# Optimization experiments

Hardware: AMD Instinct MI355X
Metric: run time of the kernel (lower is better)

Reference implementation:

```python
import jax, jax.numpy as jnp
import numpy as np

HEAD_DIM = 64
NORM_EPS = 1e-5
W_SCALE = -0.6065306597126334  # -exp(-0.5)


def _rwkv7_scan(r, w, k, v, a, b):
    # r,w,k,a,b: [B,T,H,K]; v: [B,T,H,V]. Official RWKV7 recurrence (per head):
    #   S_t = S_{t-1} * diag(exp(w_t)) + (S_{t-1} @ a_t) b_t^T + v_t k_t^T ,  o_t = S_t @ r_t
    Bsz, T, H, K = r.shape
    V = v.shape[-1]
    decay = jnp.exp(w)

    def step(S, xs):
        r_t, d_t, k_t, v_t, a_t, b_t = xs
        sa = jnp.einsum('bhvk,bhk->bhv', S, a_t)
        S = S * d_t[:, :, None, :] + sa[..., None] * b_t[:, :, None, :] + v_t[..., None] * k_t[:, :, None, :]
        o_t = jnp.einsum('bhvk,bhk->bhv', S, r_t)
        return S, o_t

    xs = tuple(jnp.moveaxis(t, 1, 0) for t in (r, decay, k, v, a, b))
    S0 = jnp.zeros((Bsz, H, V, K), dtype=r.dtype)
    _, o = jax.lax.scan(step, S0, xs)
    return jnp.moveaxis(o, 0, 1)  # [B,T,H,V]


def setup_inputs() -> dict:
    key = jax.random.key(0)
    B, T, H = 2, 4096, 2048
    NH, DK, DV = 32, 64, 64
    D_DECAY, D_A, D_V, D_G = 96, 96, 64, 256
    ks = iter(jax.random.split(key, 40))
    n = lambda *s: jax.random.normal(next(ks), s, dtype=jnp.float32)
    u = lambda *s: jax.random.uniform(next(ks), s, dtype=jnp.float32)
    inp = {
        'hidden_states': n(B, T, H),
        'v_first': n(B, T, H),
        'x_r': u(1, 1, H), 'x_w': u(1, 1, H), 'x_k': u(1, 1, H),
        'x_v': u(1, 1, H), 'x_a': u(1, 1, H), 'x_g': u(1, 1, H),
        'k_k': 0.71 + 0.05 * n(H),
        'k_a': 1.02 + 0.05 * n(H),
        'r_k': -0.04 + 0.02 * n(NH, DK),
        'w_r': 0.02 * n(H, H), 'w_k': 0.002 * n(H, H),
        'w_v': 0.02 * n(H, H), 'w_o': 0.02 * n(H, H),
        'wA': 0.02 * n(D_DECAY, H), 'wB': 0.02 * n(H, D_DECAY), 'wb': -0.5 + 0.1 * n(H),
        'aA': 0.02 * n(D_A, H), 'aB': 0.02 * n(H, D_A), 'ab': 0.1 * n(H),
        'vA': 0.02 * n(D_V, H), 'vB': 0.02 * n(H, D_V), 'vb': 0.5 + 0.1 * n(H),
        'gA': 0.02 * n(D_G, H), 'gB': 0.02 * n(H, D_G),
        'gn_w': jnp.ones(H, jnp.float32),
        'gn_b': jnp.zeros(H, jnp.float32),
    }
    return inp


def reference(hidden_states, v_first, x_r, x_w, x_k, x_v, x_a, x_g,
              k_k, k_a, r_k, w_r, w_k, w_v, w_o,
              wA, wB, wb, aA, aB, ab, vA, vB, vb, gA, gB, gn_w, gn_b):
    B, T, H = hidden_states.shape
    NH, DK = r_k.shape
    DV = H // NH
    # token shift: delta = shift(x) - x (zero-padded at t=0)
    shifted = jnp.pad(hidden_states, ((0, 0), (1, 0), (0, 0)))[:, :-1]
    delta = shifted - hidden_states
    xr = hidden_states + delta * x_r
    xw = hidden_states + delta * x_w
    xk = hidden_states + delta * x_k
    xv = hidden_states + delta * x_v
    xa = hidden_states + delta * x_a
    xg = hidden_states + delta * x_g
    r = xr @ w_r.T
    w = W_SCALE * jax.nn.sigmoid(jnp.tanh(xw @ wA.T) @ wB.T + wb)  # log-decay in (-0.6065, 0)
    k = xk @ w_k.T
    v = xv @ w_v.T
    v = v + (v_first - v) * jax.nn.sigmoid((xv @ vA.T) @ vB.T + vb)  # lerp with v_first (layer_idx != 0)
    a = jax.nn.sigmoid((xa @ aA.T) @ aB.T + ab)
    g = jax.nn.sigmoid(xg @ gA.T) @ gB.T  # g_lora: sigmoid activation inside, no bias
    kk = (k * k_k).reshape(B, T, NH, DK)
    kk = kk / jnp.maximum(jnp.linalg.norm(kk, axis=-1, keepdims=True), 1e-12)
    k = k * (1.0 + (a - 1.0) * k_a)  # fused_k_rwkv7
    r4 = r.reshape(B, T, NH, DK)
    w4 = w.reshape(B, T, NH, DK)
    k4 = k.reshape(B, T, NH, DK)
    a4 = a.reshape(B, T, NH, DK)
    v4 = v.reshape(B, T, NH, DV)
    o = _rwkv7_scan(r4, w4, k4, v4, -kk, kk * a4)  # [B,T,NH,DV]
    # GroupNorm over each head (eps = head_dim * norm_eps)
    mu = o.mean(-1, keepdims=True)
    var = ((o - mu) ** 2).mean(-1, keepdims=True)
    on = (o - mu) / jnp.sqrt(var + HEAD_DIM * NORM_EPS)
    on = on * gn_w.reshape(NH, DV) + gn_b.reshape(NH, DV)
    on = on + (r4 * k4 * r_k).sum(-1, keepdims=True) * v4
    out = (on.reshape(B, T, H) * g) @ w_o.T
    return out
```

## Files before the change

kernel.cpp:

```cpp
#include <hip/hip_runtime.h>
#include <cstdint>
#include <cstddef>

typedef unsigned short u16;
typedef unsigned int u32;

typedef __bf16 bf8_t __attribute__((ext_vector_type(8)));
typedef float f4_t __attribute__((ext_vector_type(4)));

__device__ __forceinline__ u16 f2bf(float x) {
  u32 u = __float_as_uint(x);
  u = (u + 0x7fffu + ((u >> 16) & 1u)) >> 16;
  return (u16)u;
}
__device__ __forceinline__ float bf2f(u16 x) {
  u32 u = ((u32)x) << 16;
  return __uint_as_float(u);
}
__device__ __forceinline__ float sigf(float x) { return 1.f / (1.f + __expf(-x)); }

#define MFMA16(a, b, c) __builtin_amdgcn_mfma_f32_16x16x32_bf16(a, b, c, 0, 0, 0)

__global__ void fill_kernel(float* p, float v, long n) {
  long i = (long)blockIdx.x * blockDim.x + threadIdx.x;
  if (i < n) p[i] = v;
}

__global__ void padcvt_kernel(const float* __restrict__ src, u16* __restrict__ dst,
                              int rows, int cols, int pc, long total) {
  long i = (long)blockIdx.x * blockDim.x + threadIdx.x;
  if (i >= total) return;
  int r = (int)(i / pc), c = (int)(i % pc);
  float v = (r < rows && c < cols) ? src[(long)r * cols + c] : 0.f;
  dst[i] = f2bf(v);
}

__global__ void wf_kernel(const float* __restrict__ src, const float* __restrict__ coef,
                          u16* __restrict__ Wf, int rows_valid, int row0, long total) {
  long i = (long)blockIdx.x * blockDim.x + threadIdx.x;
  if (i >= total) return;
  int r = (int)(i >> 12);
  int k = (int)(i & 4095);
  float v = 0.f;
  if (r < rows_valid) {
    int kk = k & 2047;
    v = src[(long)r * 2048 + kk];
    if (k >= 2048) v *= coef[kk];
  }
  Wf[(long)(row0 + r) * 4096 + k] = f2bf(v);
}

__global__ void wab_kernel(const float* __restrict__ wB, const float* __restrict__ aB,
                           u16* __restrict__ Wab, long total) {
  long i = (long)blockIdx.x * blockDim.x + threadIdx.x;
  if (i >= total) return;
  int r = (int)(i >> 8), k = (int)(i & 255);
  float v = 0.f;
  if (r < 2048) { if (k < 96) v = wB[(long)r * 96 + k]; }
  else { int rr = r - 2048; if (k >= 128 && k < 224) v = aB[(long)rr * 96 + (k - 128)]; }
  Wab[i] = f2bf(v);
}

__global__ void hd_kernel(const float* __restrict__ h_b, u16* __restrict__ out_seg,
                          int t0, int Tc, long total4) {
  long i = (long)blockIdx.x * blockDim.x + threadIdx.x;
  if (i >= total4) return;
  long e = i * 4;
  const int H = 2048;
  int col = (int)(e % H);
  int tl = (int)(e / H);
  int tg = t0 + tl;
  const float* hp = h_b + (long)tg * H + col;
  float4 hv = *(const float4*)hp;
  float4 pv = make_float4(0.f, 0.f, 0.f, 0.f);
  if (tg > 0) pv = *(const float4*)(hp - H);
  u16* row = out_seg + (long)tl * 4096;
  uint2 ph, pd;
  ph.x = (u32)f2bf(hv.x) | ((u32)f2bf(hv.y) << 16);
  ph.y = (u32)f2bf(hv.z) | ((u32)f2bf(hv.w) << 16);
  pd.x = (u32)f2bf(pv.x - hv.x) | ((u32)f2bf(pv.y - hv.y) << 16);
  pd.y = (u32)f2bf(pv.z - hv.z) | ((u32)f2bf(pv.w - hv.w) << 16);
  *(uint2*)(row + col) = ph;
  *(uint2*)(row + 2048 + col) = pd;
}

__global__ void mix1_kernel(const float* __restrict__ h_b, const float* __restrict__ coef,
                            u16* __restrict__ out_seg, int t0, int Tc, long total4) {
  long i = (long)blockIdx.x * blockDim.x + threadIdx.x;
  if (i >= total4) return;
  long e = i * 4;
  const int H = 2048;
  int col = (int)(e % H);
  int tl = (int)(e / H);
  int tg = t0 + tl;
  const float* hp = h_b + (long)tg * H + col;
  float4 hv = *(const float4*)hp;
  float4 pv = make_float4(0.f, 0.f, 0.f, 0.f);
  if (tg > 0) pv = *(const float4*)(hp - H);
  float4 cc = *(const float4*)(coef + col);
  uint2 pk;
  pk.x = (u32)f2bf(hv.x + (pv.x - hv.x) * cc.x) | ((u32)f2bf(hv.y + (pv.y - hv.y) * cc.y) << 16);
  pk.y = (u32)f2bf(hv.z + (pv.z - hv.z) * cc.z) | ((u32)f2bf(hv.w + (pv.w - hv.w) * cc.w) << 16);
  *(uint2*)(out_seg + e) = pk;
}

#define LDSW 40
template <int MODE>
__global__ __launch_bounds__(256) void gemm_bt(
    const u16* __restrict__ A, const u16* __restrict__ B, void* __restrict__ Cv,
    int M, int N, int K, int lda, const float* __restrict__ aux1) {
  __shared__ u16 sA[128 * LDSW];
  __shared__ u16 sB[128 * LDSW];
  const int tid = threadIdx.x;
  const long bm = (long)blockIdx.y * 128;
  const long bn = (long)blockIdx.x * 128;
  const int wave = tid >> 6, lane = tid & 63;
  const int wm = (wave >> 1) * 64, wn = (wave & 1) * 64;
  const int quad = lane >> 4, rr = lane & 15;

  f4_t acc[4][4];
  const f4_t zero = {0.f, 0.f, 0.f, 0.f};
#pragma unroll
  for (int i = 0; i < 4; i++)
#pragma unroll
    for (int j = 0; j < 4; j++) acc[i][j] = zero;

  const int c0 = tid, c1 = tid + 256;
  const u16* pa0 = A + (bm + (c0 >> 2)) * (long)lda + (c0 & 3) * 8;
  const u16* pa1 = A + (bm + (c1 >> 2)) * (long)lda + (c1 & 3) * 8;
  const u16* pb0 = B + (bn + (c0 >> 2)) * (long)K + (c0 & 3) * 8;
  const u16* pb1 = B + (bn + (c1 >> 2)) * (long)K + (c1 & 3) * 8;

  uint4 a0A, a1A, b0A, b1A, a0B, a1B, b0B, b1B;
#define LDGA(k0)                            \
  {                                         \
    a0A = *(const uint4*)(pa0 + (k0));      \
    a1A = *(const uint4*)(pa1 + (k0));      \
    b0A = *(const uint4*)(pb0 + (k0));      \
    b1A = *(const uint4*)(pb1 + (k0));      \
  }
#define LDGB(k0)                            \
  {                                         \
    a0B = *(const uint4*)(pa0 + (k0));      \
    a1B = *(const uint4*)(pa1 + (k0));      \
    b0B = *(const uint4*)(pb0 + (k0));      \
    b1B = *(const uint4*)(pb1 + (k0));      \
  }
#define STLDS(ra0, ra1, rb0, rb1)                          \
  {                                                        \
    *(uint4*)(&sA[(c0 >> 2) * LDSW + (c0 & 3) * 8]) = ra0; \
    *(uint4*)(&sA[(c1 >> 2) * LDSW + (c1 & 3) * 8]) = ra1; \
    *(uint4*)(&sB[(c0 >> 2) * LDSW + (c0 & 3) * 8]) = rb0; \
    *(uint4*)(&sB[(c1 >> 2) * LDSW + (c1 & 3) * 8]) = rb1; \
  }
#define COMPUTE                                                        \
  {                                                                    \
    bf8_t af[4], bfv[4];                                               \
    _Pragma("unroll") for (int i = 0; i < 4; i++)                      \
        af[i] = *(const bf8_t*)(&sA[(wm + i * 16 + rr) * LDSW + quad * 8]); \
    _Pragma("unroll") for (int j = 0; j < 4; j++)                      \
        bfv[j] = *(const bf8_t*)(&sB[(wn + j * 16 + rr) * LDSW + quad * 8]); \
    _Pragma("unroll") for (int i = 0; i < 4; i++)                      \
        _Pragma("unroll") for (int j = 0; j < 4; j++)                  \
            acc[i][j] = MFMA16(af[i], bfv[j], acc[i][j]);              \
  }

  LDGA(0);
  LDGB(32);
  for (int k0 = 0; k0 < K; k0 += 64) {
    __syncthreads();
    STLDS(a0A, a1A, b0A, b1A);
    __syncthreads();
    if (k0 + 64 < K) LDGA(k0 + 64);
    COMPUTE;
    __syncthreads();
    STLDS(a0B, a1B, b0B, b1B);
    __syncthreads();
    if (k0 + 96 < K) LDGB(k0 + 96);
    COMPUTE;
  }
#undef LDGA
#undef LDGB
#undef STLDS
#undef COMPUTE
#pragma unroll
  for (int i = 0; i < 4; i++)
#pragma unroll
    for (int j = 0; j < 4; j++)
#pragma unroll
      for (int rg = 0; rg < 4; rg++) {
        long m = bm + wm + i * 16 + quad * 4 + rg;
        long n = bn + wn + j * 16 + rr;
        long id = m * (long)N + n;
        float x = acc[i][j][rg];
        if (MODE == 0) ((float*)Cv)[id] = x;
        else if (MODE == 1) ((u16*)Cv)[id] = f2bf(x);
        else if (MODE == 2) ((u16*)Cv)[id] = f2bf(tanhf(x));
        else if (MODE == 3) ((u16*)Cv)[id] = f2bf(sigf(x));
        else if (MODE == 5) {
          float y = (n < 128) ? tanhf(x) : ((n < 384) ? x : sigf(x));
          ((u16*)Cv)[id] = f2bf(y);
        } else if (MODE == 6) {
          ((u16*)Cv)[id] = f2bf(sigf(x + aux1[(int)n]));
        }
      }
}

__device__ __forceinline__ void gload16(const u16* g, u16* l) {
  __builtin_amdgcn_global_load_lds((const __attribute__((address_space(1))) u32*)g,
                                   (__attribute__((address_space(3))) u32*)l, 16, 0, 0);
}

template <int MODE>
__global__ __launch_bounds__(512, 2) void gemm256_bt(
    const u16* __restrict__ A, const u16* __restrict__ Bw, void* __restrict__ Cv,
    int M, int N, int K, int rsp, long r0off, long r1off) {
  __shared__ u16 L[2][2][2][8192];
  const int tid = threadIdx.x;
  const int lane = tid & 63, w = tid >> 6;
  const int quad = lane >> 4, l15 = lane & 15;
  const long bm = (long)blockIdx.y * 256, bn = (long)blockIdx.x * 256;
  const int wm = (w >> 2) * 128, wn = (w & 3) * 64;
  const int NT = K >> 6;

  const int u0 = tid, u1 = tid + 512;
  const int ar0 = u0 >> 2, ar1 = u1 >> 2;
  const int aq0 = (u0 & 3) ^ (ar0 & 3), aq1 = (u1 & 3) ^ (ar1 & 3);
  const u16* gA0 = A + (bm + ar0) * (long)K + aq0 * 8;
  const u16* gA1 = A + (bm + ar1) * (long)K + aq1 * 8;
  const u16* gB0 = Bw + (bn + ar0) * (long)K + aq0 * 8;
  const u16* gB1 = Bw + (bn + ar1) * (long)K + aq1 * 8;

  const int qx = (quad ^ (l15 & 3)) * 8;
  const int roA = (wm + l15) * 32 + qx;
  const int roB = (wn + l15) * 32 + qx;

  f4_t acc[8][4];
#pragma unroll
  for (int i = 0; i < 8; i++)
#pragma unroll
    for (int j = 0; j < 4; j++) acc[i][j] = (f4_t){0.f, 0.f, 0.f, 0.f};

#define STG_A(buf, s, tt)                                   \
  {                                                         \
    long ko = ((long)(tt) << 6) + ((s) << 5);               \
    gload16(gA0 + ko, &L[buf][0][s][u0 * 8]);               \
    gload16(gA1 + ko, &L[buf][0][s][u1 * 8]);               \
  }
#define STG_B(buf, s, tt)                                   \
  {                                                         \
    long ko = ((long)(tt) << 6) + ((s) << 5);               \
    gload16(gB0 + ko, &L[buf][1][s][u0 * 8]);               \
    gload16(gB1 + ko, &L[buf][1][s][u1 * 8]);               \
  }
#define LDA4(P, o)                                          \
  _Pragma("unroll") for (int i = 0; i < 4; i++)             \
      aF[i] = *(const bf8_t*)((P) + roA + ((o) + i) * 512);
#define LDB4(P)                                             \
  _Pragma("unroll") for (int j = 0; j < 4; j++)             \
      bF[j] = *(const bf8_t*)((P) + roB + j * 512);
#define MFMA_BLK(base)                                      \
  __builtin_amdgcn_s_setprio(1);                            \
  _Pragma("unroll") for (int i = 0; i < 4; i++)             \
      _Pragma("unroll") for (int j = 0; j < 4; j++)         \
          acc[(base) + i][j] = MFMA16(aF[i], bF[j], acc[(base) + i][j]); \
  __builtin_amdgcn_s_setprio(0);
#define SBAR __builtin_amdgcn_s_barrier()

  STG_A(0, 0, 0); STG_B(0, 0, 0);
  STG_A(0, 1, 0); STG_B(0, 1, 0);
  if (NT > 1) { STG_A(1, 0, 1); STG_B(1, 0, 1); }
  asm volatile("s_waitcnt vmcnt(8)" ::: "memory");
  SBAR;

  bf8_t aF[4], bF[4];
  for (int t = 0; t < NT; ++t) {
    const int buf = t & 1;
    const u16* A0 = &L[buf][0][0][0];
    const u16* B0 = &L[buf][1][0][0];
    const u16* A1 = &L[buf][0][1][0];
    const u16* B1 = &L[buf][1][1][0];
    LDA4(A0, 0);
    LDB4(B0);
    if (t + 1 < NT) STG_A(buf ^ 1, 1, t + 1);
    SBAR;
    asm volatile("s_waitcnt lgkmcnt(0)" ::: "memory");
    MFMA_BLK(0);
    SBAR;
    LDA4(A0, 4);
    if (t + 1 < NT) STG_B(buf ^ 1, 1, t + 1);
    SBAR;
    asm volatile("s_waitcnt lgkmcnt(0)" ::: "memory");
    MFMA_BLK(4);
    if (t == NT - 1) asm volatile("s_waitcnt vmcnt(0)" ::: "memory");
    else asm volatile("s_waitcnt vmcnt(8)" ::: "memory");
    SBAR;
    LDA4(A1, 0);
    LDB4(B1);
    if (t + 2 < NT) STG_A(buf, 0, t + 2);
    SBAR;
    asm volatile("s_waitcnt lgkmcnt(0)" ::: "memory");
    MFMA_BLK(0);
    SBAR;
    LDA4(A1, 4);
    if (t + 2 < NT) STG_B(buf, 0, t + 2);
    SBAR;
    asm volatile("s_waitcnt lgkmcnt(0)" ::: "memory");
    MFMA_BLK(4);
    if (t == NT - 2) asm volatile("s_waitcnt vmcnt(4)" ::: "memory");
    else if (t < NT - 2) asm volatile("s_waitcnt vmcnt(8)" ::: "memory");
    SBAR;
  }

#pragma unroll
  for (int i = 0; i < 8; i++) {
#pragma unroll
    for (int rg = 0; rg < 4; rg++) {
      long mm = bm + wm + i * 16 + quad * 4 + rg;
      long crow = (mm < rsp) ? (mm + r0off) : (mm + r1off);
#pragma unroll
      for (int j = 0; j < 4; j++) {
        long n = bn + wn + j * 16 + l15;
        float x = acc[i][j][rg];
        if (MODE == 0) ((float*)Cv)[crow * (long)N + n] = x;
        else ((u16*)Cv)[crow * (long)N + n] = f2bf(x);
      }
    }
  }
#undef STG_A
#undef STG_B
#undef LDA4
#undef LDB4
#undef MFMA_BLK
#undef SBAR
}

__global__ __launch_bounds__(256) void post1_kernel(
    const float* __restrict__ F1, const float* __restrict__ F0F4, float* __restrict__ W,
    const float* __restrict__ F2, const u16* __restrict__ VL,
    const float* __restrict__ vfirst,
    u16* __restrict__ KM, u16* __restrict__ KK, u16* __restrict__ BB, u16* __restrict__ VB,
    const float* __restrict__ k_k, const float* __restrict__ k_a,
    const float* __restrict__ wb, const float* __restrict__ ab, int t0, int Tc) {
  const int lane = threadIdx.x & 63;
  const long th = (((long)blockIdx.x * 256) + threadIdx.x) >> 6;
  const int hcol = (int)(th & 31) * 64 + lane;
  const long idx = th * 64 + lane;
  const long r = th >> 5;
  float kraw = F1[idx];
  float kk0 = kraw * k_k[hcol];
  float ss = kk0 * kk0;
#pragma unroll
  for (int m = 32; m; m >>= 1) ss += __shfl_xor(ss, m, 64);
  float kkn = kk0 / fmaxf(sqrtf(ss), 1e-12f);
  float wlog = F0F4[r * 4096 + hcol];
  float alog = F0F4[r * 4096 + 2048 + hcol];
  float av = sigf(alog + ab[hcol]);
  float w = -0.6065306597126334f * sigf(wlog + wb[hcol]);
  W[idx] = w;
  KM[idx] = f2bf(kraw * (1.f + (av - 1.f) * k_a[hcol]));
  KK[idx] = f2bf(kkn);
  BB[idx] = f2bf(kkn * av);
  float vraw = F2[idx];
  float sg = bf2f(VL[idx]);
  long vfi = ((r / Tc) * 4096 + t0 + (r % Tc)) * 2048 + hcol;
  VB[idx] = f2bf(vraw + (vfirst[vfi] - vraw) * sg);
}

constexpr int ST64 = 72;
constexpr int ST32 = 40;
constexpr int STX = 132;

__global__ __launch_bounds__(64) void phaseA_kernel(
    const float* __restrict__ wS, const u16* __restrict__ kmS, const u16* __restrict__ kkS,
    const u16* __restrict__ bbS, const u16* __restrict__ vbS, const u16* __restrict__ rbS,
    float* __restrict__ POWb, u16* __restrict__ PAb, float* __restrict__ Zb,
    u16* __restrict__ GTb, float* __restrict__ CLb, int Tc, int sp0) {
  __shared__ u16 lXa[16 * ST64], lXr[16 * ST64], lYa[16 * ST64], lYb[16 * ST64];
  __shared__ u16 lYaT[64 * ST32], lYbT[64 * ST32], lVmT[64 * ST32];
  __shared__ u16 lTWt[64 * ST32], lTAt[64 * ST32];
  __shared__ u16 lP[16 * ST32], lQ[16 * ST32], lBm[16 * ST32];
  __shared__ float lA[16 * 16];
  __shared__ float lX[16 * STX];
  __shared__ float lcl[64];
  const int lane = threadIdx.x;
  const int quad = lane >> 4, l15 = lane & 15;
  const long tile = blockIdx.x;
  const int bh = (int)(tile & 63);
  const int col = (int)(tile >> 6);
  const int b = bh >> 5, h = bh & 31;
  const long s = tile;
  const f4_t z4 = {0.f, 0.f, 0.f, 0.f};

  {
    u32* p0 = (u32*)&lYaT[lane * ST32 + 16];
    u32* p1 = (u32*)&lYbT[lane * ST32 + 16];
    u32* p2 = (u32*)&lVmT[lane * ST32 + 16];
    u32* p3 = (u32*)&lTWt[lane * ST32 + 16];
    u32* p4 = (u32*)&lTAt[lane * ST32 + 16];
#pragma unroll
    for (int q = 0; q < 8; q++) { p0[q] = 0; p1[q] = 0; p2[q] = 0; p3[q] = 0; p4[q] = 0; }
    if (lane < 16) {
      u32* q0 = (u32*)&lP[lane * ST32 + 16];
      u32* q1 = (u32*)&lQ[lane * ST32 + 16];
      u32* q2 = (u32*)&lBm[lane * ST32 + 16];
#pragma unroll
      for (int q = 0; q < 8; q++) { q0[q] = 0; q1[q] = 0; q2[q] = 0; }
    }
  }

  const long rowbase = (long)b * Tc + (long)(sp0 + col) * 16;
  const long gbase = rowbase * 2048 + (long)h * 64 + lane;
  float cw = 0.f;
#pragma unroll
  for (int i = 0; i < 16; i++) {
    long g = gbase + (long)i * 2048;
    float w = wS[g];
    float km = bf2f(kmS[g]), kk = bf2f(kkS[g]), bb = bf2f(bbS[g]);
    float vv = bf2f(vbS[g]), rr2 = bf2f(rbS[g]);
    float cwm = cw;
    cw += w;
    float E1 = __expf(cwm), E2 = __expf(-cw), E3 = __expf(cw);
    float xa = -kk * E1;
    lXa[i * ST64 + lane] = f2bf(xa);
    lX[i * STX + 64 + lane] = xa;
    lXr[i * ST64 + lane] = f2bf(rr2 * E3);
    float ya = bb * E2, yb = km * E2;
    lYa[i * ST64 + lane] = f2bf(ya);
    lYb[i * ST64 + lane] = f2bf(yb);
    lYaT[lane * ST32 + i] = f2bf(ya);
    lYbT[lane * ST32 + i] = f2bf(yb);
    lVmT[lane * ST32 + i] = f2bf(vv);
    if (i == 15) { lcl[lane] = E3; CLb[s * 64 + lane] = E3; }
  }
  __syncthreads();

  {
    f4_t aA = z4, aB = z4, aP = z4, aQ = z4;
#pragma unroll
    for (int kc = 0; kc < 2; kc++) {
      bf8_t xa = *(const bf8_t*)&lXa[l15 * ST64 + quad * 8 + 32 * kc];
      bf8_t xr = *(const bf8_t*)&lXr[l15 * ST64 + quad * 8 + 32 * kc];
      bf8_t ya = *(const bf8_t*)&lYa[l15 * ST64 + quad * 8 + 32 * kc];
      bf8_t yb = *(const bf8_t*)&lYb[l15 * ST64 + quad * 8 + 32 * kc];
      aA = MFMA16(xa, ya, aA);
      aB = MFMA16(xa, yb, aB);
      aP = MFMA16(xr, ya, aP);
      aQ = MFMA16(xr, yb, aQ);
    }
#pragma unroll
    for (int rg = 0; rg < 4; rg++) {
      int m = quad * 4 + rg;
      lA[m * 16 + l15] = (l15 < m) ? aA[rg] : 0.f;
      lBm[m * ST32 + l15] = (l15 < m) ? f2bf(aB[rg]) : (u16)0;
      lP[m * ST32 + l15] = (l15 <= m) ? f2bf(aP[rg]) : (u16)0;
      lQ[m * ST32 + l15] = (l15 <= m) ? f2bf(aQ[rg]) : (u16)0;
    }
  }
  __syncthreads();

#pragma unroll
  for (int nt = 0; nt < 4; nt++) {
    f4_t acc = z4;
    bf8_t a = *(const bf8_t*)&lBm[l15 * ST32 + quad * 8];
    bf8_t bb2 = *(const bf8_t*)&lVmT[(nt * 16 + l15) * ST32 + quad * 8];
    acc = MFMA16(a, bb2, acc);
#pragma unroll
    for (int rg = 0; rg < 4; rg++) lX[(quad * 4 + rg) * STX + nt * 16 + l15] = acc[rg];
  }
  __syncthreads();

  for (int i = 1; i < 16; i++) {
    float x0 = lX[i * STX + lane], x1 = lX[i * STX + 64 + lane];
    for (int j = 0; j < i; j++) {
      float aij = lA[i * 16 + j];
      x0 += aij * lX[j * STX + lane];
      x1 += aij * lX[j * STX + 64 + lane];
    }
    lX[i * STX + lane] = x0;
    lX[i * STX + 64 + lane] = x1;
  }
#pragma unroll
  for (int i = 0; i < 16; i++) {
    lTWt[lane * ST32 + i] = f2bf(lX[i * STX + lane]);
    lTAt[lane * ST32 + i] = f2bf(lX[i * STX + 64 + lane]);
  }
  __syncthreads();

#pragma unroll
  for (int nt = 0; nt < 4; nt++) {
    f4_t acc = z4;
    bf8_t p = *(const bf8_t*)&lP[l15 * ST32 + quad * 8];
    bf8_t q = *(const bf8_t*)&lQ[l15 * ST32 + quad * 8];
    bf8_t tw = *(const bf8_t*)&lTWt[(nt * 16 + l15) * ST32 + quad * 8];
    bf8_t vm = *(const bf8_t*)&lVmT[(nt * 16 + l15) * ST32 + quad * 8];
    acc = MFMA16(p, tw, acc);
    acc = MFMA16(q, vm, acc);
#pragma unroll
    for (int rg = 0; rg < 4; rg++)
      POWb[s * 1024 + (quad * 4 + rg) * 64 + nt * 16 + l15] = acc[rg];
  }
#pragma unroll
  for (int nt = 0; nt < 4; nt++) {
    f4_t acc = z4;
    bf8_t p = *(const bf8_t*)&lP[l15 * ST32 + quad * 8];
    bf8_t ta = *(const bf8_t*)&lTAt[(nt * 16 + l15) * ST32 + quad * 8];
    acc = MFMA16(p, ta, acc);
#pragma unroll
    for (int rg = 0; rg < 4; rg++) {
      float xr = bf2f(lXr[(quad * 4 + rg) * ST64 + nt * 16 + l15]);
      PAb[s * 1024 + (quad * 4 + rg) * 64 + nt * 16 + l15] = f2bf(acc[rg] + xr);
    }
  }

#pragma unroll
  for (int mt = 0; mt < 4; mt++)
#pragma unroll
    for (int nt = 0; nt < 4; nt++) {
      f4_t acc = z4;
      bf8_t tw = *(const bf8_t*)&lTWt[(mt * 16 + l15) * ST32 + quad * 8];
      bf8_t vm = *(const bf8_t*)&lVmT[(mt * 16 + l15) * ST32 + quad * 8];
      bf8_t yat = *(const bf8_t*)&lYaT[(nt * 16 + l15) * ST32 + quad * 8];
      bf8_t ybt = *(const bf8_t*)&lYbT[(nt * 16 + l15) * ST32 + quad * 8];
      acc = MFMA16(tw, yat, acc);
      acc = MFMA16(vm, ybt, acc);
      float cl = lcl[nt * 16 + l15];
#pragma unroll
      for (int rg = 0; rg < 4; rg++)
        Zb[s * 4096 + (mt * 16 + quad * 4 + rg) * 64 + nt * 16 + l15] = acc[rg] * cl;
    }
#pragma unroll
  for (int mt = 0; mt < 4; mt++)
#pragma unroll
    for (int nt = 0; nt < 4; nt++) {
      f4_t acc = z4;
      bf8_t yat = *(const bf8_t*)&lYaT[(mt * 16 + l15) * ST32 + quad * 8];
      bf8_t ta = *(const bf8_t*)&lTAt[(nt * 16 + l15) * ST32 + quad * 8];
      acc = MFMA16(yat, ta, acc);
#pragma unroll
      for (int rg = 0; rg < 4; rg++) {
        float cl = lcl[mt * 16 + quad * 4 + rg];
        GTb[s * 4096 + (mt * 16 + quad * 4 + rg) * 64 + nt * 16 + l15] = f2bf(acc[rg] * cl);
      }
    }
}

__global__ __launch_bounds__(256) void phaseB_kernel(
    const float* __restrict__ Zb, const u16* __restrict__ GTb, const float* __restrict__ CLb,
    u16* __restrict__ S0b, float* __restrict__ state, int CT, int init) {
  __shared__ u16 Sb[64 * ST64];
  const int bh = blockIdx.x;
  const int tid = threadIdx.x, wv = tid >> 6, lane = tid & 63;
  const int quad = lane >> 4, l15 = lane & 15;
  float S[4][4];
  if (init) {
#pragma unroll
    for (int nt = 0; nt < 4; nt++)
#pragma unroll
      for (int rg = 0; rg < 4; rg++) S[nt][rg] = 0.f;
  } else {
#pragma unroll
    for (int nt = 0; nt < 4; nt++)
#pragma unroll
      for (int rg = 0; rg < 4; rg++)
        S[nt][rg] = state[(long)bh * 4096 + (16 * wv + quad * 4 + rg) * 64 + nt * 16 + l15];
  }
  const f4_t z4 = {0.f, 0.f, 0.f, 0.f};

  uint4 gtA[2][4], gtB[2][4];
  float zA[4][4], zB[4][4], clA[4], clB[4];

#define LOADSET(cc, gt, z, cl)                                                      \
  {                                                                                 \
    long s2 = (long)(cc) * 64 + bh;                                                 \
    _Pragma("unroll") for (int kc = 0; kc < 2; kc++)                                \
        _Pragma("unroll") for (int nt = 0; nt < 4; nt++)                            \
            gt[kc][nt] = *(const uint4*)(GTb + s2 * 4096 + (nt * 16 + l15) * 64 + quad * 8 + 32 * kc); \
    _Pragma("unroll") for (int nt = 0; nt < 4; nt++) {                              \
      cl[nt] = CLb[s2 * 64 + nt * 16 + l15];                                        \
      _Pragma("unroll") for (int rg = 0; rg < 4; rg++)                              \
          z[nt][rg] = Zb[s2 * 4096 + (16 * wv + quad * 4 + rg) * 64 + nt * 16 + l15]; \
    }                                                                               \
  }
#define BSTEP(cc, gt, z, cl, gtN, zN, clN, pf)                                      \
  {                                                                                 \
    long s1 = (long)(cc) * 64 + bh;                                                 \
    _Pragma("unroll") for (int nt = 0; nt < 4; nt++)                                \
        _Pragma("unroll") for (int rg = 0; rg < 4; rg++)                            \
            Sb[(16 * wv + quad * 4 + rg) * ST64 + nt * 16 + l15] = f2bf(S[nt][rg]); \
    __syncthreads();                                                                \
    if (pf) LOADSET((cc) + 1, gtN, zN, clN);                                        \
    f4_t acc[4] = {z4, z4, z4, z4};                                                 \
    _Pragma("unroll") for (int kc = 0; kc < 2; kc++) {                              \
      bf8_t a = *(const bf8_t*)&Sb[(16 * wv + l15) * ST64 + quad * 8 + 32 * kc];    \
      *(uint4*)(S0b + s1 * 4096 + (16 * wv + l15) * 64 + quad * 8 + 32 * kc) = *(uint4*)&a; \
      _Pragma("unroll") for (int nt = 0; nt < 4; nt++) {                            \
        bf8_t g = *(const bf8_t*)&gt[kc][nt];                                       \
        acc[nt] = MFMA16(a, g, acc[nt]);                                            \
      }                                                                             \
    }                                                                               \
    _Pragma("unroll") for (int nt = 0; nt < 4; nt++)                                \
        _Pragma("unroll") for (int rg = 0; rg < 4; rg++)                            \
            S[nt][rg] = S[nt][rg] * cl[nt] + acc[nt][rg] + z[nt][rg];               \
    __syncthreads();                                                                \
  }

  LOADSET(0, gtA, zA, clA);
  for (int c = 0; c < CT; c += 2) {
    BSTEP(c, gtA, zA, clA, gtB, zB, clB, (c + 1 < CT));
    BSTEP(c + 1, gtB, zB, clB, gtA, zA, clA, (c + 2 < CT));
  }
#undef LOADSET
#undef BSTEP
#pragma unroll
  for (int nt = 0; nt < 4; nt++)
#pragma unroll
    for (int rg = 0; rg < 4; rg++)
      state[(long)bh * 4096 + (16 * wv + quad * 4 + rg) * 64 + nt * 16 + l15] = S[nt][rg];
}

__global__ __launch_bounds__(64) void phaseC_kernel(
    const float* __restrict__ POWb, const u16* __restrict__ PAb, const u16* __restrict__ S0b,
    float* __restrict__ O, int Tc, int sp0) {
  const int lane = threadIdx.x, quad = lane >> 4, l15 = lane & 15;
  const long tile = blockIdx.x;
  const int bh = (int)(tile & 63), col = (int)(tile >> 6);
  const int b = bh >> 5, h = bh & 31;
  const long s = tile;
  const f4_t z4 = {0.f, 0.f, 0.f, 0.f};
  f4_t acc[4] = {z4, z4, z4, z4};
#pragma unroll
  for (int kc = 0; kc < 2; kc++) {
    bf8_t a = *(const bf8_t*)(PAb + s * 1024 + l15 * 64 + quad * 8 + 32 * kc);
#pragma unroll
    for (int nt = 0; nt < 4; nt++) {
      bf8_t bo = *(const bf8_t*)(S0b + s * 4096 + (nt * 16 + l15) * 64 + quad * 8 + 32 * kc);
      acc[nt] = MFMA16(a, bo, acc[nt]);
    }
  }
  const long rowbase = (long)b * Tc + (long)(sp0 + col) * 16;
#pragma unroll
  for (int nt = 0; nt < 4; nt++)
#pragma unroll
    for (int rg = 0; rg < 4; rg++) {
      int i = quad * 4 + rg, v = nt * 16 + l15;
      float p = POWb[s * 1024 + i * 64 + v];
      O[(rowbase + i) * 2048 + (long)h * 64 + v] = p + acc[nt][rg];
    }
}

__global__ __launch_bounds__(256) void epi_kernel(
    const float* __restrict__ o, const u16* __restrict__ r, const u16* __restrict__ k,
    const u16* __restrict__ v, const u16* __restrict__ g,
    const float* __restrict__ r_k, const float* __restrict__ gn_w, const float* __restrict__ gn_b,
    u16* __restrict__ y) {
  const int lane = threadIdx.x & 63;
  const long th = (((long)blockIdx.x * 256) + threadIdx.x) >> 6;
  const int hcol = (int)(th & 31) * 64 + lane;
  const long idx = th * 64 + lane;
  float ov = o[idx];
  float s = ov;
#pragma unroll
  for (int m = 32; m; m >>= 1) s += __shfl_xor(s, m, 64);
  float mu = s * (1.f / 64.f);
  float d = ov - mu;
  float vs = d * d;
#pragma unroll
  for (int m = 32; m; m >>= 1) vs += __shfl_xor(vs, m, 64);
  float on = d * rsqrtf(vs * (1.f / 64.f) + 6.4e-4f);
  on = on * gn_w[hcol] + gn_b[hcol];
  float rk = bf2f(r[idx]) * bf2f(k[idx]) * r_k[hcol];
#pragma unroll
  for (int m = 32; m; m >>= 1) rk += __shfl_xor(rk, m, 64);
  on += rk * bf2f(v[idx]);
  y[idx] = f2bf(on * bf2f(g[idx]));
}

extern "C" void kernel_launch(void* const* d_in, const int* in_sizes, int n_in,
                              void* d_out, int out_size, void* d_ws, size_t ws_size,
                              hipStream_t stream) {
  constexpr int B = 2, T = 4096, H = 2048;
  const float* hst    = (const float*)d_in[0];
  const float* vfirst = (const float*)d_in[1];
  const float* x_r = (const float*)d_in[2];
  const float* x_w = (const float*)d_in[3];
  const float* x_k = (const float*)d_in[4];
  const float* x_v = (const float*)d_in[5];
  const float* x_a = (const float*)d_in[6];
  const float* x_g = (const float*)d_in[7];
  const float* k_k = (const float*)d_in[8];
  const float* k_a = (const float*)d_in[9];
  const float* r_k = (const float*)d_in[10];
  const float* w_r = (const float*)d_in[11];
  const float* w_k = (const float*)d_in[12];
  const float* w_v = (const float*)d_in[13];
  const float* w_o = (const float*)d_in[14];
  const float* wA  = (const float*)d_in[15];
  const float* wB  = (const float*)d_in[16];
  const float* wb  = (const float*)d_in[17];
  const float* aA  = (const float*)d_in[18];
  const float* aB  = (const float*)d_in[19];
  const float* ab  = (const float*)d_in[20];
  const float* vA  = (const float*)d_in[21];
  const float* vB  = (const float*)d_in[22];
  const float* vb  = (const float*)d_in[23];
  const float* gA  = (const float*)d_in[24];
  const float* gB  = (const float*)d_in[25];
  const float* gn_w= (const float*)d_in[26];
  const float* gn_b= (const float*)d_in[27];

  const size_t WEIGHT_BYTES = 4 * (size_t)H * H * 2 + (size_t)H * 128 * 2
                            + (size_t)H * 256 * 2 + (size_t)768 * 4096 * 2
                            + (size_t)4096 * 256 * 2;
  const size_t STATE_BYTES = (size_t)64 * 4096 * 4;
  const size_t TILE_BYTES = 4096 + 2048 + 16384 + 8192 + 256 + 8192;

  int NC = -1, CT = 0;
  for (int pass = 0; pass < 2 && NC < 0; pass++) {
    for (int nc : {1, 2, 4, 8, 16}) {
      long Tc_ = T / nc;
      long R_ = (long)B * Tc_;
      long RH_ = R_ * H;
      size_t base = (size_t)RH_ * 40 + (size_t)R_ * 1536
                  + WEIGHT_BYTES + STATE_BYTES + (4 << 20);
      int cols = (int)(Tc_ / 16);
      int found = 0;
      for (int ct : {64, 32, 16, 8}) {
        if (ct > cols) continue;
        if (pass == 0 && ct < 16) continue;
        size_t need = base + (size_t)64 * ct * TILE_BYTES;
        if (need <= ws_size) { NC = nc; CT = ct; found = 1; break; }
      }
      if (found) break;
    }
  }
  const int BS = 256;
  auto cdiv = [](long a, long b) { return (int)((a + b - 1) / b); };
  if (NC < 0) {
    fill_kernel<<<cdiv(out_size, BS), BS, 0, stream>>>(
        (float*)d_out, 200000.f + (float)(ws_size >> 20), out_size);
    return;
  }
  const int Tc = T / NC;
  const long R = (long)B * Tc;
  const long RH = R * H;
  const int cols = Tc / 16;
  const int NTILE = 64 * CT;

  char* ws = (char*)d_ws;
  size_t off = 0;
  auto alloc = [&](size_t bytes) -> void* {
    void* p = ws + off;
    off += (bytes + 255) & ~(size_t)255;
    return p;
  };
  float* F0F4 = (float*)alloc(RH * 8);
  float* F1 = (float*)alloc(RH * 4);
  float* F2 = (float*)alloc(RH * 4);
  float* W  = (float*)alloc(RH * 4);
  u16* KM  = (u16*)alloc(RH * 2);
  u16* KK  = (u16*)alloc(RH * 2);
  u16* BBs = (u16*)alloc(RH * 2);
  u16* VBs = (u16*)alloc(RH * 2);
  u16* RBs = (u16*)alloc(RH * 2);
  u16* MIXB = (u16*)alloc(RH * 2);
  u16* G    = (u16*)alloc(RH * 2);
  u16* VL   = (u16*)alloc(RH * 2);
  u16* HD   = (u16*)alloc(RH * 4);
  u16* s1all = (u16*)alloc(R * 1536);
  u16* wrb = (u16*)alloc((size_t)H * H * 2);
  u16* wkb = (u16*)alloc((size_t)H * H * 2);
  u16* wvb = (u16*)alloc((size_t)H * H * 2);
  u16* wob = (u16*)alloc((size_t)H * H * 2);
  u16* vBb = (u16*)alloc((size_t)H * 128 * 2);
  u16* gBb = (u16*)alloc((size_t)H * 256 * 2);
  u16* Wf  = (u16*)alloc((size_t)768 * 4096 * 2);
  u16* Wab = (u16*)alloc((size_t)4096 * 256 * 2);
  float* state = (float*)alloc(STATE_BYTES);
  float* POWb = (float*)alloc((size_t)NTILE * 4096);
  u16*   PAb  = (u16*)alloc((size_t)NTILE * 2048);
  float* Zb   = (float*)alloc((size_t)NTILE * 16384);
  u16*   GTb  = (u16*)alloc((size_t)NTILE * 8192);
  float* CLb  = (float*)alloc((size_t)NTILE * 256);
  u16*   S0b  = (u16*)alloc((size_t)NTILE * 8192);
  float* Ob = F1;

  padcvt_kernel<<<cdiv((long)H * H, BS), BS, 0, stream>>>(w_r, wrb, H, H, H, (long)H * H);
  padcvt_kernel<<<cdiv((long)H * H, BS), BS, 0, stream>>>(w_k, wkb, H, H, H, (long)H * H);
  padcvt_kernel<<<cdiv((long)H * H, BS), BS, 0, stream>>>(w_v, wvb, H, H, H, (long)H * H);
  padcvt_kernel<<<cdiv((long)H * H, BS), BS, 0, stream>>>(w_o, wob, H, H, H, (long)H * H);
  padcvt_kernel<<<cdiv((long)H * 128, BS), BS, 0, stream>>>(vB, vBb, H, 64, 128, (long)H * 128);
  padcvt_kernel<<<cdiv((long)H * 256, BS), BS, 0, stream>>>(gB, gBb, H, 256, 256, (long)H * 256);
  wf_kernel<<<cdiv((long)128 * 4096, BS), BS, 0, stream>>>(wA, x_w, Wf, 96, 0, (long)128 * 4096);
  wf_kernel<<<cdiv((long)128 * 4096, BS), BS, 0, stream>>>(aA, x_a, Wf, 96, 128, (long)128 * 4096);
  wf_kernel<<<cdiv((long)128 * 4096, BS), BS, 0, stream>>>(vA, x_v, Wf, 64, 256, (long)128 * 4096);
  wf_kernel<<<cdiv((long)384 * 4096, BS), BS, 0, stream>>>(gA, x_g, Wf, 256, 384, (long)384 * 4096);
  wab_kernel<<<cdiv((long)4096 * 256, BS), BS, 0, stream>>>(wB, aB, Wab, (long)4096 * 256);

  const long mixTot = (long)Tc * H / 4;
  const int mixG = cdiv(mixTot, BS);
  const int ehG = (int)(R * 32 / 4);

  for (int c = 0; c < NC; c++) {
    const int t0 = c * Tc;
    auto MIX = [&](const float* coef) {
      for (int b = 0; b < B; b++)
        mix1_kernel<<<mixG, BS, 0, stream>>>(hst + (long)b * T * H, coef,
                                             MIXB + (long)b * Tc * H, t0, Tc, mixTot);
    };
    dim3 gBig(16, (unsigned)(R / 128)), gF(6, (unsigned)(R / 128)), gWA(32, (unsigned)(R / 128));
    dim3 g256((unsigned)(H / 256), (unsigned)(R / 256));

    for (int b = 0; b < B; b++)
      hd_kernel<<<mixG, BS, 0, stream>>>(hst + (long)b * T * H,
                                         HD + (long)b * Tc * 4096, t0, Tc, mixTot);
    gemm_bt<5><<<gF, 256, 0, stream>>>(HD, Wf, s1all, (int)R, 768, 4096, 4096, nullptr);
    gemm_bt<0><<<gWA, 256, 0, stream>>>(s1all, Wab, F0F4, (int)R, 4096, 256, 768, nullptr);
    MIX(x_v);
    gemm256_bt<0><<<g256, 512, 0, stream>>>(MIXB, wvb, F2, (int)R, H, H, (int)R, 0, 0);
    gemm_bt<6><<<gBig, 256, 0, stream>>>(s1all + 256, vBb, VL, (int)R, H, 128, 768, vb);
    gemm_bt<1><<<gBig, 256, 0, stream>>>(s1all + 384, gBb, G, (int)R, H, 256, 768, nullptr);
    MIX(x_r);
    gemm256_bt<1><<<g256, 512, 0, stream>>>(MIXB, wrb, RBs, (int)R, H, H, (int)R, 0, 0);
    MIX(x_k);
    gemm256_bt<0><<<g256, 512, 0, stream>>>(MIXB, wkb, F1, (int)R, H, H, (int)R, 0, 0);
    post1_kernel<<<ehG, 256, 0, stream>>>(F1, F0F4, W, F2, VL, vfirst,
                                          KM, KK, BBs, VBs, k_k, k_a, wb, ab, t0, Tc);
    for (int sp = 0; sp < cols; sp += CT) {
      phaseA_kernel<<<NTILE, 64, 0, stream>>>(W, KM, KK, BBs, VBs, RBs,
                                              POWb, PAb, Zb, GTb, CLb, Tc, sp);
      phaseB_kernel<<<64, 256, 0, stream>>>(Zb, GTb, CLb, S0b, state, CT,
                                            (c == 0 && sp == 0) ? 1 : 0);
      phaseC_kernel<<<NTILE, 64, 0, stream>>>(POWb, PAb, S0b, Ob, Tc, sp);
    }
    epi_kernel<<<ehG, 256, 0, stream>>>(Ob, RBs, KM, VBs, G, r_k, gn_w, gn_b, MIXB);
    gemm256_bt<0><<<g256, 512, 0, stream>>>(MIXB, wob, (float*)d_out, (int)R, H, H,
                                            Tc, (long)t0, (long)T - Tc + t0);
  }
}
```

Measured before the change: 2.745 ms.

## Fuse token-shift mixes, merge v/g LoRA GEMMs, fold group-norm epilogue into phaseC

Replaces the separate hd and three mix kernels with one kernel that reads hidden states once and writes HD plus the v/r/k mixed inputs. It trims the g-LoRA first projection from 384 to 256 padded columns and merges the vB and gB second-stage GEMMs into one launch with a split epilogue. The per-head GroupNorm, r*k bonus and gating epilogue moves into the phaseC kernel, so the fp32 O buffer is no longer written and re-read. It also raises the allowed chunk tile counts to 256 and 128, at the cost of more memory for the extra mix buffers and larger tiles.

```diff
diff --git a/kernel.cpp b/kernel.cpp
--- a/kernel.cpp
+++ b/kernel.cpp
@@ -61,8 +61,23 @@
   Wab[i] = f2bf(v);
 }
 
-__global__ void hd_kernel(const float* __restrict__ h_b, u16* __restrict__ out_seg,
-                          int t0, int Tc, long total4) {
+__global__ void wvg_kernel(const float* __restrict__ vB, const float* __restrict__ gB,
+                           u16* __restrict__ Wvg, long total) {
+  long i = (long)blockIdx.x * blockDim.x + threadIdx.x;
+  if (i >= total) return;
+  int r = (int)(i / 384), k = (int)(i % 384);
+  float v = 0.f;
+  if (r < 2048) { if (k < 64) v = vB[(long)r * 64 + k]; }
+  else { if (k >= 128) v = gB[(long)(r - 2048) * 256 + (k - 128)]; }
+  Wvg[i] = f2bf(v);
+}
+
+__global__ void mixhd_kernel(const float* __restrict__ h_b,
+                             const float* __restrict__ xv, const float* __restrict__ xr,
+                             const float* __restrict__ xk,
+                             u16* __restrict__ HD, u16* __restrict__ MV,
+                             u16* __restrict__ MR, u16* __restrict__ MK,
+                             int t0, long total4) {
   long i = (long)blockIdx.x * blockDim.x + threadIdx.x;
   if (i >= total4) return;
   long e = i * 4;
@@ -74,41 +89,35 @@
   float4 hv = *(const float4*)hp;
   float4 pv = make_float4(0.f, 0.f, 0.f, 0.f);
   if (tg > 0) pv = *(const float4*)(hp - H);
-  u16* row = out_seg + (long)tl * 4096;
+  float dx = pv.x - hv.x, dy = pv.y - hv.y, dz = pv.z - hv.z, dw = pv.w - hv.w;
+  u16* hrow = HD + (long)tl * 4096;
   uint2 ph, pd;
   ph.x = (u32)f2bf(hv.x) | ((u32)f2bf(hv.y) << 16);
   ph.y = (u32)f2bf(hv.z) | ((u32)f2bf(hv.w) << 16);
-  pd.x = (u32)f2bf(pv.x - hv.x) | ((u32)f2bf(pv.y - hv.y) << 16);
-  pd.y = (u32)f2bf(pv.z - hv.z) | ((u32)f2bf(pv.w - hv.w) << 16);
-  *(uint2*)(row + col) = ph;
-  *(uint2*)(row + 2048 + col) = pd;
-}
-
-__global__ void mix1_kernel(const float* __restrict__ h_b, const float* __restrict__ coef,
-                            u16* __restrict__ out_seg, int t0, int Tc, long total4) {
-  long i = (long)blockIdx.x * blockDim.x + threadIdx.x;
-  if (i >= total4) return;
-  long e = i * 4;
-  const int H = 2048;
-  int col = (int)(e % H);
-  int tl = (int)(e / H);
-  int tg = t0 + tl;
-  const float* hp = h_b + (long)tg * H + col;
-  float4 hv = *(const float4*)hp;
-  float4 pv = make_float4(0.f, 0.f, 0.f, 0.f);
-  if (tg > 0) pv = *(const float4*)(hp - H);
-  float4 cc = *(const float4*)(coef + col);
-  uint2 pk;
-  pk.x = (u32)f2bf(hv.x + (pv.x - hv.x) * cc.x) | ((u32)f2bf(hv.y + (pv.y - hv.y) * cc.y) << 16);
-  pk.y = (u32)f2bf(hv.z + (pv.z - hv.z) * cc.z) | ((u32)f2bf(hv.w + (pv.w - hv.w) * cc.w) << 16);
-  *(uint2*)(out_seg + e) = pk;
+  pd.x = (u32)f2bf(dx) | ((u32)f2bf(dy) << 16);
+  pd.y = (u32)f2bf(dz) | ((u32)f2bf(dw) << 16);
+  *(uint2*)(hrow + col) = ph;
+  *(uint2*)(hrow + 2048 + col) = pd;
+  float4 cv = *(const float4*)(xv + col);
+  float4 cr = *(const float4*)(xr + col);
+  float4 ck = *(const float4*)(xk + col);
+  uint2 mv, mr, mk;
+  mv.x = (u32)f2bf(hv.x + dx * cv.x) | ((u32)f2bf(hv.y + dy * cv.y) << 16);
+  mv.y = (u32)f2bf(hv.z + dz * cv.z) | ((u32)f2bf(hv.w + dw * cv.w) << 16);
+  mr.x = (u32)f2bf(hv.x + dx * cr.x) | ((u32)f2bf(hv.y + dy * cr.y) << 16);
+  mr.y = (u32)f2bf(hv.z + dz * cr.z) | ((u32)f2bf(hv.w + dw * cr.w) << 16);
+  mk.x = (u32)f2bf(hv.x + dx * ck.x) | ((u32)f2bf(hv.y + dy * ck.y) << 16);
+  mk.y = (u32)f2bf(hv.z + dz * ck.z) | ((u32)f2bf(hv.w + dw * ck.w) << 16);
+  *(uint2*)(MV + e) = mv;
+  *(uint2*)(MR + e) = mr;
+  *(uint2*)(MK + e) = mk;
 }
 
 #define LDSW 40
 template <int MODE>
 __global__ __launch_bounds__(256) void gemm_bt(
     const u16* __restrict__ A, const u16* __restrict__ B, void* __restrict__ Cv,
-    int M, int N, int K, int lda, const float* __restrict__ aux1) {
+    int M, int N, int K, int lda, const float* __restrict__ aux1, void* __restrict__ Cv2) {
   __shared__ u16 sA[128 * LDSW];
   __shared__ u16 sB[128 * LDSW];
   const int tid = threadIdx.x;
@@ -191,17 +200,14 @@
       for (int rg = 0; rg < 4; rg++) {
         long m = bm + wm + i * 16 + quad * 4 + rg;
         long n = bn + wn + j * 16 + rr;
-        long id = m * (long)N + n;
         float x = acc[i][j][rg];
-        if (MODE == 0) ((float*)Cv)[id] = x;
-        else if (MODE == 1) ((u16*)Cv)[id] = f2bf(x);
-        else if (MODE == 2) ((u16*)Cv)[id] = f2bf(tanhf(x));
-        else if (MODE == 3) ((u16*)Cv)[id] = f2bf(sigf(x));
+        if (MODE == 0) ((float*)Cv)[m * (long)N + n] = x;
         else if (MODE == 5) {
           float y = (n < 128) ? tanhf(x) : ((n < 384) ? x : sigf(x));
-          ((u16*)Cv)[id] = f2bf(y);
-        } else if (MODE == 6) {
-          ((u16*)Cv)[id] = f2bf(sigf(x + aux1[(int)n]));
+          ((u16*)Cv)[m * (long)N + n] = f2bf(y);
+        } else if (MODE == 8) {
+          if (n < 2048) ((u16*)Cv)[m * 2048 + n] = f2bf(sigf(x + aux1[(int)n]));
+          else ((u16*)Cv2)[m * 2048 + (n - 2048)] = f2bf(x);
         }
       }
 }
@@ -619,9 +625,12 @@
       state[(long)bh * 4096 + (16 * wv + quad * 4 + rg) * 64 + nt * 16 + l15] = S[nt][rg];
 }
 
-__global__ __launch_bounds__(64) void phaseC_kernel(
+__global__ __launch_bounds__(64) void phaseCE_kernel(
     const float* __restrict__ POWb, const u16* __restrict__ PAb, const u16* __restrict__ S0b,
-    float* __restrict__ O, int Tc, int sp0) {
+    const u16* __restrict__ RBs, const u16* __restrict__ KMs, const u16* __restrict__ VBs,
+    const u16* __restrict__ Gs, const float* __restrict__ r_k,
+    const float* __restrict__ gn_w, const float* __restrict__ gn_b,
+    u16* __restrict__ Y, int Tc, int sp0) {
   const int lane = threadIdx.x, quad = lane >> 4, l15 = lane & 15;
   const long tile = blockIdx.x;
   const int bh = (int)(tile & 63), col = (int)(tile >> 6);
@@ -639,41 +648,50 @@
     }
   }
   const long rowbase = (long)b * Tc + (long)(sp0 + col) * 16;
+  float o_[4][4];
 #pragma unroll
   for (int nt = 0; nt < 4; nt++)
 #pragma unroll
+    for (int rg = 0; rg < 4; rg++)
+      o_[nt][rg] = POWb[s * 1024 + (quad * 4 + rg) * 64 + nt * 16 + l15] + acc[nt][rg];
+  const int hcl = h * 64 + lane;
+  const float rkw = r_k[hcl];
+  float rk4[4];
+#pragma unroll
+  for (int i = 0; i < 16; i++) {
+    long gi = (rowbase + i) * 2048 + hcl;
+    float p = bf2f(RBs[gi]) * bf2f(KMs[gi]) * rkw;
+#pragma unroll
+    for (int m = 32; m; m >>= 1) p += __shfl_xor(p, m, 64);
+    if ((i >> 2) == quad) rk4[i & 3] = p;
+  }
+  float mu[4], ri[4];
+#pragma unroll
+  for (int rg = 0; rg < 4; rg++) {
+    float ssum = o_[0][rg] + o_[1][rg] + o_[2][rg] + o_[3][rg];
+#pragma unroll
+    for (int m = 8; m; m >>= 1) ssum += __shfl_xor(ssum, m, 64);
+    mu[rg] = ssum * (1.f / 64.f);
+    float vs = 0.f;
+#pragma unroll
+    for (int nt = 0; nt < 4; nt++) { float d = o_[nt][rg] - mu[rg]; vs += d * d; }
+#pragma unroll
+    for (int m = 8; m; m >>= 1) vs += __shfl_xor(vs, m, 64);
+    ri[rg] = rsqrtf(vs * (1.f / 64.f) + 6.4e-4f);
+  }
+#pragma unroll
+  for (int nt = 0; nt < 4; nt++) {
+    int hcv = h * 64 + nt * 16 + l15;
+    float gw = gn_w[hcv], gb = gn_b[hcv];
+#pragma unroll
     for (int rg = 0; rg < 4; rg++) {
-      int i = quad * 4 + rg, v = nt * 16 + l15;
-      float p = POWb[s * 1024 + i * 64 + v];
-      O[(rowbase + i) * 2048 + (long)h * 64 + v] = p + acc[nt][rg];
-    }
-}
-
-__global__ __launch_bounds__(256) void epi_kernel(
-    const float* __restrict__ o, const u16* __restrict__ r, const u16* __restrict__ k,
-    const u16* __restrict__ v, const u16* __restrict__ g,
-    const float* __restrict__ r_k, const float* __restrict__ gn_w, const float* __restrict__ gn_b,
-    u16* __restrict__ y) {
-  const int lane = threadIdx.x & 63;
-  const long th = (((long)blockIdx.x * 256) + threadIdx.x) >> 6;
-  const int hcol = (int)(th & 31) * 64 + lane;
-  const long idx = th * 64 + lane;
-  float ov = o[idx];
-  float s = ov;
-#pragma unroll
-  for (int m = 32; m; m >>= 1) s += __shfl_xor(s, m, 64);
-  float mu = s * (1.f / 64.f);
-  float d = ov - mu;
-  float vs = d * d;
-#pragma unroll
-  for (int m = 32; m; m >>= 1) vs += __shfl_xor(vs, m, 64);
-  float on = d * rsqrtf(vs * (1.f / 64.f) + 6.4e-4f);
-  on = on * gn_w[hcol] + gn_b[hcol];
-  float rk = bf2f(r[idx]) * bf2f(k[idx]) * r_k[hcol];
-#pragma unroll
-  for (int m = 32; m; m >>= 1) rk += __shfl_xor(rk, m, 64);
-  on += rk * bf2f(v[idx]);
-  y[idx] = f2bf(on * bf2f(g[idx]));
+      long gi = (rowbase + quad * 4 + rg) * 2048 + hcv;
+      float on = (o_[nt][rg] - mu[rg]) * ri[rg];
+      on = on * gw + gb;
+      on += rk4[rg] * bf2f(VBs[gi]);
+      Y[gi] = f2bf(on * bf2f(Gs[gi]));
+    }
+  }
 }
 
 extern "C" void kernel_launch(void* const* d_in, const int* in_sizes, int n_in,
@@ -709,9 +727,8 @@
   const float* gn_w= (const float*)d_in[26];
   const float* gn_b= (const float*)d_in[27];
 
-  const size_t WEIGHT_BYTES = 4 * (size_t)H * H * 2 + (size_t)H * 128 * 2
-                            + (size_t)H * 256 * 2 + (size_t)768 * 4096 * 2
-                            + (size_t)4096 * 256 * 2;
+  const size_t WEIGHT_BYTES = 4 * (size_t)H * H * 2 + (size_t)640 * 4096 * 2
+                            + (size_t)4096 * 256 * 2 + (size_t)4096 * 384 * 2;
   const size_t STATE_BYTES = (size_t)64 * 4096 * 4;
   const size_t TILE_BYTES = 4096 + 2048 + 16384 + 8192 + 256 + 8192;
 
@@ -721,11 +738,11 @@
       long Tc_ = T / nc;
       long R_ = (long)B * Tc_;
       long RH_ = R_ * H;
-      size_t base = (size_t)RH_ * 40 + (size_t)R_ * 1536
-                  + WEIGHT_BYTES + STATE_BYTES + (4 << 20);
+      size_t base = (size_t)RH_ * 44 + (size_t)R_ * 1280
+                  + WEIGHT_BYTES + STATE_BYTES + (8 << 20);
       int cols = (int)(Tc_ / 16);
       int found = 0;
-      for (int ct : {64, 32, 16, 8}) {
+      for (int ct : {256, 128, 64, 32, 16, 8}) {
         if (ct > cols) continue;
         if (pass == 0 && ct < 16) continue;
         size_t need = base + (size_t)64 * ct * TILE_BYTES;
@@ -763,19 +780,20 @@
   u16* BBs = (u16*)alloc(RH * 2);
   u16* VBs = (u16*)alloc(RH * 2);
   u16* RBs = (u16*)alloc(RH * 2);
-  u16* MIXB = (u16*)alloc(RH * 2);
   u16* G    = (u16*)alloc(RH * 2);
   u16* VL   = (u16*)alloc(RH * 2);
+  u16* MV   = (u16*)alloc(RH * 2);
+  u16* MR   = (u16*)alloc(RH * 2);
+  u16* MK   = (u16*)alloc(RH * 2);
   u16* HD   = (u16*)alloc(RH * 4);
-  u16* s1all = (u16*)alloc(R * 1536);
+  u16* s1all = (u16*)alloc(R * 1280);
   u16* wrb = (u16*)alloc((size_t)H * H * 2);
   u16* wkb = (u16*)alloc((size_t)H * H * 2);
   u16* wvb = (u16*)alloc((size_t)H * H * 2);
   u16* wob = (u16*)alloc((size_t)H * H * 2);
-  u16* vBb = (u16*)alloc((size_t)H * 128 * 2);
-  u16* gBb = (u16*)alloc((size_t)H * 256 * 2);
-  u16* Wf  = (u16*)alloc((size_t)768 * 4096 * 2);
+  u16* Wf  = (u16*)alloc((size_t)640 * 4096 * 2);
   u16* Wab = (u16*)alloc((size_t)4096 * 256 * 2);
+  u16* Wvg = (u16*)alloc((size_t)4096 * 384 * 2);
   float* state = (float*)alloc(STATE_BYTES);
   float* POWb = (float*)alloc((size_t)NTILE * 4096);
   u16*   PAb  = (u16*)alloc((size_t)NTILE * 2048);
@@ -783,19 +801,17 @@
   u16*   GTb  = (u16*)alloc((size_t)NTILE * 8192);
   float* CLb  = (float*)alloc((size_t)NTILE * 256);
   u16*   S0b  = (u16*)alloc((size_t)NTILE * 8192);
-  float* Ob = F1;
 
   padcvt_kernel<<<cdiv((long)H * H, BS), BS, 0, stream>>>(w_r, wrb, H, H, H, (long)H * H);
   padcvt_kernel<<<cdiv((long)H * H, BS), BS, 0, stream>>>(w_k, wkb, H, H, H, (long)H * H);
   padcvt_kernel<<<cdiv((long)H * H, BS), BS, 0, stream>>>(w_v, wvb, H, H, H, (long)H * H);
   padcvt_kernel<<<cdiv((long)H * H, BS), BS, 0, stream>>>(w_o, wob, H, H, H, (long)H * H);
-  padcvt_kernel<<<cdiv((long)H * 128, BS), BS, 0, stream>>>(vB, vBb, H, 64, 128, (long)H * 128);
-  padcvt_kernel<<<cdiv((long)H * 256, BS), BS, 0, stream>>>(gB, gBb, H, 256, 256, (long)H * 256);
   wf_kernel<<<cdiv((long)128 * 4096, BS), BS, 0, stream>>>(wA, x_w, Wf, 96, 0, (long)128 * 4096);
   wf_kernel<<<cdiv((long)128 * 4096, BS), BS, 0, stream>>>(aA, x_a, Wf, 96, 128, (long)128 * 4096);
   wf_kernel<<<cdiv((long)128 * 4096, BS), BS, 0, stream>>>(vA, x_v, Wf, 64, 256, (long)128 * 4096);
-  wf_kernel<<<cdiv((long)384 * 4096, BS), BS, 0, stream>>>(gA, x_g, Wf, 256, 384, (long)384 * 4096);
+  wf_kernel<<<cdiv((long)256 * 4096, BS), BS, 0, stream>>>(gA, x_g, Wf, 256, 384, (long)256 * 4096);
   wab_kernel<<<cdiv((long)4096 * 256, BS), BS, 0, stream>>>(wB, aB, Wab, (long)4096 * 256);
+  wvg_kernel<<<cdiv((long)4096 * 384, BS), BS, 0, stream>>>(vB, gB, Wvg, (long)4096 * 384);
 
   const long mixTot = (long)Tc * H / 4;
   const int mixG = cdiv(mixTot, BS);
@@ -803,27 +819,24 @@
 
   for (int c = 0; c < NC; c++) {
     const int t0 = c * Tc;
-    auto MIX = [&](const float* coef) {
-      for (int b = 0; b < B; b++)
-        mix1_kernel<<<mixG, BS, 0, stream>>>(hst + (long)b * T * H, coef,
-                                             MIXB + (long)b * Tc * H, t0, Tc, mixTot);
-    };
-    dim3 gBig(16, (unsigned)(R / 128)), gF(6, (unsigned)(R / 128)), gWA(32, (unsigned)(R / 128));
+    dim3 gF(5, (unsigned)(R / 128)), gWA(32, (unsigned)(R / 128)), gVG(32, (unsigned)(R / 128));
     dim3 g256((unsigned)(H / 256), (unsigned)(R / 256));
 
     for (int b = 0; b < B; b++)
-      hd_kernel<<<mixG, BS, 0, stream>>>(hst + (long)b * T * H,
-                                         HD + (long)b * Tc * 4096, t0, Tc, mixTot);
-    gemm_bt<5><<<gF, 256, 0, stream>>>(HD, Wf, s1all, (int)R, 768, 4096, 4096, nullptr);
-    gemm_bt<0><<<gWA, 256, 0, stream>>>(s1all, Wab, F0F4, (int)R, 4096, 256, 768, nullptr);
-    MIX(x_v);
-    gemm256_bt<0><<<g256, 512, 0, stream>>>(MIXB, wvb, F2, (int)R, H, H, (int)R, 0, 0);
-    gemm_bt<6><<<gBig, 256, 0, stream>>>(s1all + 256, vBb, VL, (int)R, H, 128, 768, vb);
-    gemm_bt<1><<<gBig, 256, 0, stream>>>(s1all + 384, gBb, G, (int)R, H, 256, 768, nullptr);
-    MIX(x_r);
-    gemm256_bt<1><<<g256, 512, 0, stream>>>(MIXB, wrb, RBs, (int)R, H, H, (int)R, 0, 0);
-    MIX(x_k);
-    gemm256_bt<0><<<g256, 512, 0, stream>>>(MIXB, wkb, F1, (int)R, H, H, (int)R, 0, 0);
+      mixhd_kernel<<<mixG, BS, 0, stream>>>(hst + (long)b * T * H, x_v, x_r, x_k,
+                                            HD + (long)b * Tc * 4096,
+                                            MV + (long)b * Tc * H,
+                                            MR + (long)b * Tc * H,
+                                            MK + (long)b * Tc * H, t0, mixTot);
+    gemm_bt<5><<<gF, 256, 0, stream>>>(HD, Wf, s1all, (int)R, 640, 4096, 4096,
+                                       nullptr, nullptr);
+    gemm_bt<0><<<gWA, 256, 0, stream>>>(s1all, Wab, F0F4, (int)R, 4096, 256, 640,
+                                        nullptr, nullptr);
+    gemm256_bt<0><<<g256, 512, 0, stream>>>(MV, wvb, F2, (int)R, H, H, (int)R, 0, 0);
+    gemm_bt<8><<<gVG, 256, 0, stream>>>(s1all + 256, Wvg, VL, (int)R, 4096, 384, 640,
+                                        vb, G);
+    gemm256_bt<1><<<g256, 512, 0, stream>>>(MR, wrb, RBs, (int)R, H, H, (int)R, 0, 0);
+    gemm256_bt<0><<<g256, 512, 0, stream>>>(MK, wkb, F1, (int)R, H, H, (int)R, 0, 0);
     post1_kernel<<<ehG, 256, 0, stream>>>(F1, F0F4, W, F2, VL, vfirst,
                                           KM, KK, BBs, VBs, k_k, k_a, wb, ab, t0, Tc);
     for (int sp = 0; sp < cols; sp += CT) {
@@ -831,10 +844,10 @@
                                               POWb, PAb, Zb, GTb, CLb, Tc, sp);
       phaseB_kernel<<<64, 256, 0, stream>>>(Zb, GTb, CLb, S0b, state, CT,
                                             (c == 0 && sp == 0) ? 1 : 0);
-      phaseC_kernel<<<NTILE, 64, 0, stream>>>(POWb, PAb, S0b, Ob, Tc, sp);
-    }
-    epi_kernel<<<ehG, 256, 0, stream>>>(Ob, RBs, KM, VBs, G, r_k, gn_w, gn_b, MIXB);
-    gemm256_bt<0><<<g256, 512, 0, stream>>>(MIXB, wob, (float*)d_out, (int)R, H, H,
+      phaseCE_kernel<<<NTILE, 64, 0, stream>>>(POWb, PAb, S0b, RBs, KM, VBs, G,
+                                               r_k, gn_w, gn_b, MV, Tc, sp);
+    }
+    gemm256_bt<0><<<g256, 512, 0, stream>>>(MV, wob, (float*)d_out, (int)R, H, H,
                                             Tc, (long)t0, (long)T - Tc + t0);
   }
 }
```

New measurement: 3.802 ms. 1.39x slower.
